# Kernel tuning notes

Hardware: AMD Instinct MI355X
Metric: run time of the kernel (lower is better)

## Reference

```python
import jax, jax.numpy as jnp
import numpy as np

C = 1.0      # base manifold curvature (Lorentz c)
C_E = 1.0    # expert manifold curvature (all experts init to c=1.0)
K = 1        # n_activated_experts (top-k)
SCALE = 2.0  # LResNet scale for shared-expert combine
EPS = 1e-8


def _lorentz_swiglu(x, W1, W3, W2, c_mid, c_out, prescale):
    """LorentzExpert / LorentzFeedForward: SwiGLU on space coords with Lorentz time lift.
    x: [T, D] (full Lorentz vector). W1,W3: [I-1, D]; W2: [D-1, I]. Returns [T, D]."""
    if prescale:
        x = x * np.float32(np.sqrt(C_E / C))  # x * sqrt(c_expert / c)
    s1 = jax.nn.silu(x @ W1.T)                 # [T, I-1] w1(x, return_space=True)
    s3 = x @ W3.T                              # [T, I-1] w3(x, return_space=True)
    sp = s1 * s3                               # gated space part
    t = jnp.sqrt(jnp.clip((sp * sp).sum(-1, keepdims=True) + c_mid, EPS))
    h = jnp.concatenate([t, sp], axis=-1)      # [T, I] point on expert manifold
    o = h @ W2.T                               # [T, D-1] w2 space output
    ot = jnp.sqrt(jnp.clip((o * o).sum(-1, keepdims=True) + c_out, EPS))
    return jnp.concatenate([ot, o], axis=-1)   # [T, D] on base manifold


def setup_inputs() -> dict:
    key = jax.random.key(0)
    ks = jax.random.split(key, 9)
    T, D, E, I = 2048, 1024, 8, 1024
    x = jax.random.normal(ks[0], (T, D), jnp.float32)
    gate_w = jax.random.normal(ks[1], (E, D - 1), jnp.float32) / np.sqrt(D - 1)
    gate_b = jax.random.normal(ks[2], (E,), jnp.float32) * 0.01
    W1 = jax.random.normal(ks[3], (E, I - 1, D), jnp.float32) / np.sqrt(D)
    W3 = jax.random.normal(ks[4], (E, I - 1, D), jnp.float32) / np.sqrt(D)
    W2 = jax.random.normal(ks[5], (E, D - 1, I), jnp.float32) / np.sqrt(I)
    Ws1 = jax.random.normal(ks[6], (I - 1, D), jnp.float32) / np.sqrt(D)
    Ws3 = jax.random.normal(ks[7], (I - 1, D), jnp.float32) / np.sqrt(D)
    Ws2 = jax.random.normal(ks[8], (D - 1, I), jnp.float32) / np.sqrt(I)
    return {"x": x, "gate_w": gate_w, "gate_b": gate_b, "W1": W1, "W3": W3,
            "W2": W2, "Ws1": Ws1, "Ws3": Ws3, "Ws2": Ws2}


def reference(x, gate_w, gate_b, W1, W3, W2, Ws1, Ws3, Ws2):
    T, D = x.shape
    E = gate_w.shape[0]
    # ---- Gate (softmax scoring, n_groups == 1, route_scale == 1.0) ----
    logits = x[:, 1:] @ gate_w.T                                    # [T, E]
    scores = jax.nn.softmax(logits.astype(jnp.float32), axis=-1)
    biased = scores + gate_b                                        # bias only affects routing
    _, idx = jax.lax.top_k(biased, K)                               # [T, K]
    weights = jnp.take_along_axis(scores, idx, axis=-1).astype(x.dtype)  # [T, K]
    # dense per-token expert gate weights [T, E]
    oh = jax.nn.one_hot(idx, E, dtype=x.dtype)                      # [T, K, E]
    gw = (oh * weights[..., None]).sum(axis=1)                      # [T, E]
    # ---- y init: project(zeros) -> [sqrt(c), 0, ..., 0] ----
    y0 = jnp.concatenate([jnp.full((T, 1), np.sqrt(C), x.dtype),
                          jnp.zeros((T, D - 1), x.dtype)], axis=-1)
    # ---- routed experts (dense reference: every expert on every token, masked combine) ----
    e_out = jax.vmap(lambda w1, w3, w2: _lorentz_swiglu(x, w1, w3, w2, C_E, C, True))(W1, W3, W2)  # [E, T, D]
    y = y0 + jnp.einsum('te,etd->td', gw, e_out)
    # ---- shared expert (LorentzFeedForward, stays on base manifold) ----
    z = _lorentz_swiglu(x, Ws1, Ws3, Ws2, C, C, False)
    # ---- LResNet weighted sum: normalize (z + scale*y) back to manifold ----
    comb = z + SCALE * y
    li = (comb[:, 1:] ** 2).sum(-1, keepdims=True) - comb[:, :1] ** 2  # Lorentz inner <comb,comb>
    out = np.float32(np.sqrt(C)) * comb / jnp.sqrt(jnp.clip(jnp.abs(li), EPS))
    return out
```

## Files before the change

### kernel.cpp

```cpp
#include <hip/hip_runtime.h>

typedef __bf16 bf16;
typedef __attribute__((ext_vector_type(8))) __bf16 bf16x8;
typedef __attribute__((ext_vector_type(4))) float floatx4;

#define TOK 2048
#define DD  1024
#define NE  8
#define LDA 40
#define MAXSLOT 72

__device__ __forceinline__ uint4 pack_bf8(float4 a, float4 b) {
  union { bf16 h[8]; uint4 u; } p;
  p.h[0] = (bf16)a.x; p.h[1] = (bf16)a.y; p.h[2] = (bf16)a.z; p.h[3] = (bf16)a.w;
  p.h[4] = (bf16)b.x; p.h[5] = (bf16)b.y; p.h[6] = (bf16)b.z; p.h[7] = (bf16)b.w;
  return p.u;
}

__global__ __launch_bounds__(256) void gate_cvt_kernel(
    const float* __restrict__ x, const float* __restrict__ gate_w,
    const float* __restrict__ gate_b, bf16* __restrict__ x_bf,
    int* __restrict__ eidx, float* __restrict__ ewgt)
{
  const int t = blockIdx.x, tid = threadIdx.x;
  const float4 v = ((const float4*)(x + (size_t)t * DD))[tid];
  union { bf16 h[4]; uint2 u; } pk;
  pk.h[0] = (bf16)v.x; pk.h[1] = (bf16)v.y; pk.h[2] = (bf16)v.z; pk.h[3] = (bf16)v.w;
  ((uint2*)(x_bf + (size_t)t * DD))[tid] = pk.u;

  float acc[NE];
#pragma unroll
  for (int e = 0; e < NE; ++e) acc[e] = 0.f;
  const float vv[4] = {v.x, v.y, v.z, v.w};
#pragma unroll
  for (int i = 0; i < 4; ++i) {
    const int d = tid * 4 + i;
    if (d >= 1) {
#pragma unroll
      for (int e = 0; e < NE; ++e) acc[e] += vv[i] * gate_w[e * (DD - 1) + d - 1];
    }
  }
#pragma unroll
  for (int off = 32; off > 0; off >>= 1) {
#pragma unroll
    for (int e = 0; e < NE; ++e) acc[e] += __shfl_down(acc[e], off);
  }
  __shared__ float red[4][NE];
  const int wid = tid >> 6, lane = tid & 63;
  if (lane == 0) {
#pragma unroll
    for (int e = 0; e < NE; ++e) red[wid][e] = acc[e];
  }
  __syncthreads();
  if (tid == 0) {
    float lg[NE];
#pragma unroll
    for (int e = 0; e < NE; ++e) lg[e] = red[0][e] + red[1][e] + red[2][e] + red[3][e];
    float m = lg[0];
    for (int e = 1; e < NE; ++e) m = fmaxf(m, lg[e]);
    float ex[NE], s = 0.f;
    for (int e = 0; e < NE; ++e) { ex[e] = expf(lg[e] - m); s += ex[e]; }
    const float inv = 1.f / s;
    int best = 0; float bb = ex[0] * inv + gate_b[0];
    for (int e = 1; e < NE; ++e) {
      const float b = ex[e] * inv + gate_b[e];
      if (b > bb) { bb = b; best = e; }
    }
    eidx[t] = best;
    ewgt[t] = ex[best] * inv;
  }
}

__global__ __launch_bounds__(256) void route_kernel(
    const int* __restrict__ eidx, int* __restrict__ perm,
    int* __restrict__ pos_of, int4* __restrict__ wl, int* __restrict__ wl_n)
{
  __shared__ int cnt[NE], off[NE], bas[NE + 1];
  const int tid = threadIdx.x;
  if (tid < NE) cnt[tid] = 0;
  __syncthreads();
  for (int t = tid; t < TOK; t += 256) atomicAdd(&cnt[eidx[t]], 1);
  __syncthreads();
  if (tid == 0) {
    int run = 0;
    for (int e = 0; e < NE; ++e) { bas[e] = run; off[e] = run; run += cnt[e]; }
    bas[NE] = run;
    int n = 0;
    for (int e = 0; e < NE; ++e)
      for (int r0 = 0; r0 < cnt[e]; r0 += 64) {
        int rows = cnt[e] - r0; if (rows > 64) rows = 64;
        wl[n++] = make_int4(bas[e] + r0, rows, e, 0);
      }
    for (int r0 = 0; r0 < TOK; r0 += 64) wl[n++] = make_int4(r0, 64, NE, 0);
    *wl_n = n;
  }
  __syncthreads();
  for (int t = tid; t < TOK; t += 256) {
    const int e = eidx[t];
    const int p = atomicAdd(&off[e], 1);
    perm[p] = t;
    pos_of[t] = p;
  }
}

__global__ __launch_bounds__(256) void mlp1_kernel(
    const bf16* __restrict__ x_bf,
    const float* __restrict__ W1, const float* __restrict__ W3,
    const float* __restrict__ Ws1, const float* __restrict__ Ws3,
    const int* __restrict__ perm, const int4* __restrict__ wl,
    const int* __restrict__ wl_n,
    bf16* __restrict__ h_r, bf16* __restrict__ h_s,
    float* __restrict__ ss_r, float* __restrict__ ss_z)
{
  const int bid = blockIdx.x;
  const int slot = bid >> 4, nt = bid & 15;
  if (slot >= *wl_n) return;
  const int4 wle = wl[slot];
  const int mbase = wle.x, rows = wle.y, eid = wle.z;
  const int tid = threadIdx.x;
  const bool routed = (eid < NE);
  const float* w1p = routed ? W1 + (size_t)eid * 1023 * 1024 : Ws1;
  const float* w3p = routed ? W3 + (size_t)eid * 1023 * 1024 : Ws3;
  bf16* hbuf  = routed ? h_r : h_s;
  float* ssbuf = routed ? ss_r : ss_z;
  const int n0 = nt * 64;

  __shared__ __align__(16) bf16 As[64 * LDA];
  __shared__ __align__(16) bf16 B1s[64 * LDA];
  __shared__ __align__(16) bf16 B3s[64 * LDA];
  __shared__ int toks[64];

  if (tid < 64) {
    int r = tid < rows ? tid : rows - 1;
    toks[tid] = routed ? perm[mbase + r] : (mbase + r);
  }
  __syncthreads();

  const int arow = tid >> 2, acol = (tid & 3) * 8;
  const bf16* aptr = x_bf + (size_t)toks[arow] * DD + acol;
  bf16* const alds = As + arow * LDA + acol;

  const int brow = tid >> 2, bcol = (tid & 3) * 8;
  int bn = n0 + brow; if (bn > 1022) bn = 1022;
  const float* b1ptr = w1p + (size_t)bn * 1024 + bcol;
  const float* b3ptr = w3p + (size_t)bn * 1024 + bcol;
  bf16* const b1lds = B1s + brow * LDA + bcol;
  bf16* const b3lds = B3s + brow * LDA + bcol;

  const int wid = tid >> 6, lane = tid & 63;
  const int wc = wid * 16;
  const int lrow = lane & 15, quad = lane >> 4;

  const floatx4 fz = {0.f, 0.f, 0.f, 0.f};
  floatx4 acc1[4], acc3[4];
#pragma unroll
  for (int mi = 0; mi < 4; ++mi) { acc1[mi] = fz; acc3[mi] = fz; }

  uint4  a0  = *(const uint4*)(aptr);
  float4 f10 = *(const float4*)(b1ptr);
  float4 f11 = *(const float4*)(b1ptr + 4);
  float4 f30 = *(const float4*)(b3ptr);
  float4 f31 = *(const float4*)(b3ptr + 4);

  for (int k0 = 0; k0 < 1024; k0 += 32) {
    __syncthreads();
    *(uint4*)alds  = a0;
    *(uint4*)b1lds = pack_bf8(f10, f11);
    *(uint4*)b3lds = pack_bf8(f30, f31);
    __syncthreads();
    const int kn = (k0 + 32 < 1024) ? (k0 + 32) : 0;
    a0  = *(const uint4*)(aptr + kn);
    f10 = *(const float4*)(b1ptr + kn);
    f11 = *(const float4*)(b1ptr + kn + 4);
    f30 = *(const float4*)(b3ptr + kn);
    f31 = *(const float4*)(b3ptr + kn + 4);

    bf16x8 af[4], b1f, b3f;
#pragma unroll
    for (int mi = 0; mi < 4; ++mi)
      af[mi] = *(const bf16x8*)(As + (mi * 16 + lrow) * LDA + quad * 8);
    b1f = *(const bf16x8*)(B1s + (wc + lrow) * LDA + quad * 8);
    b3f = *(const bf16x8*)(B3s + (wc + lrow) * LDA + quad * 8);
#pragma unroll
    for (int mi = 0; mi < 4; ++mi) {
      acc1[mi] = __builtin_amdgcn_mfma_f32_16x16x32_bf16(af[mi], b1f, acc1[mi], 0, 0, 0);
      acc3[mi] = __builtin_amdgcn_mfma_f32_16x16x32_bf16(af[mi], b3f, acc3[mi], 0, 0, 0);
    }
  }

  const int n = n0 + wc + lrow;
#pragma unroll
  for (int mi = 0; mi < 4; ++mi) {
#pragma unroll
    for (int r = 0; r < 4; ++r) {
      const int row = mi * 16 + quad * 4 + r;
      const bool ok = (row < rows) && (n < 1023);
      const float s1 = acc1[mi][r];
      const float s3 = acc3[mi][r];
      const float sp = (s1 / (1.f + __expf(-s1))) * s3;
      float ssum = ok ? sp * sp : 0.f;
      if (ok) hbuf[(size_t)(mbase + row) * 1024 + 1 + n] = (bf16)sp;
      ssum += __shfl_xor(ssum, 1);
      ssum += __shfl_xor(ssum, 2);
      ssum += __shfl_xor(ssum, 4);
      ssum += __shfl_xor(ssum, 8);
      if (lrow == 0 && row < rows) atomicAdd(ssbuf + mbase + row, ssum);
    }
  }
}

__global__ __launch_bounds__(256) void finalize_t_kernel(
    const float* __restrict__ ss_r, const float* __restrict__ ss_z,
    bf16* __restrict__ h_r, bf16* __restrict__ h_s)
{
  const int i = blockIdx.x * 256 + threadIdx.x;
  if (i < TOK) {
    h_r[(size_t)i * 1024] = (bf16)sqrtf(ss_r[i] + 1.0f);
    h_s[(size_t)i * 1024] = (bf16)sqrtf(ss_z[i] + 1.0f);
  }
}

__global__ __launch_bounds__(256) void mlp2_kernel(
    const bf16* __restrict__ h_r, const bf16* __restrict__ h_s,
    const float* __restrict__ W2, const float* __restrict__ Ws2,
    const int4* __restrict__ wl, const int* __restrict__ wl_n,
    float* __restrict__ o_r, float* __restrict__ o_s,
    float* __restrict__ ss_or, float* __restrict__ ss_oz)
{
  const int bid = blockIdx.x;
  const int slot = bid >> 4, nt = bid & 15;
  if (slot >= *wl_n) return;
  const int4 wle = wl[slot];
  const int mbase = wle.x, rows = wle.y, eid = wle.z;
  const int tid = threadIdx.x;
  const bool routed = (eid < NE);
  const float* wp = routed ? W2 + (size_t)eid * 1023 * 1024 : Ws2;
  const bf16* abuf = routed ? h_r : h_s;
  float* obuf  = routed ? o_r : o_s;
  float* ssbuf = routed ? ss_or : ss_oz;
  const int n0 = nt * 64;

  __shared__ __align__(16) bf16 As[64 * LDA];
  __shared__ __align__(16) bf16 Bs[64 * LDA];

  const int arow = tid >> 2, acol = (tid & 3) * 8;
  const int ar = arow < rows ? arow : rows - 1;
  const bf16* aptr = abuf + (size_t)(mbase + ar) * 1024 + acol;
  bf16* const alds = As + arow * LDA + acol;

  const int brow = tid >> 2, bcol = (tid & 3) * 8;
  int bn = n0 + brow; if (bn > 1022) bn = 1022;
  const float* bptr = wp + (size_t)bn * 1024 + bcol;
  bf16* const blds = Bs + brow * LDA + bcol;

  const int wid = tid >> 6, lane = tid & 63;
  const int wc = wid * 16;
  const int lrow = lane & 15, quad = lane >> 4;

  const floatx4 fz = {0.f, 0.f, 0.f, 0.f};
  floatx4 acc[4];
#pragma unroll
  for (int mi = 0; mi < 4; ++mi) acc[mi] = fz;

  uint4  a0 = *(const uint4*)(aptr);
  float4 f0 = *(const float4*)(bptr);
  float4 f1 = *(const float4*)(bptr + 4);

  for (int k0 = 0; k0 < 1024; k0 += 32) {
    __syncthreads();
    *(uint4*)alds = a0;
    *(uint4*)blds = pack_bf8(f0, f1);
    __syncthreads();
    const int kn = (k0 + 32 < 1024) ? (k0 + 32) : 0;
    a0 = *(const uint4*)(aptr + kn);
    f0 = *(const float4*)(bptr + kn);
    f1 = *(const float4*)(bptr + kn + 4);

    bf16x8 af[4], bfr;
#pragma unroll
    for (int mi = 0; mi < 4; ++mi)
      af[mi] = *(const bf16x8*)(As + (mi * 16 + lrow) * LDA + quad * 8);
    bfr = *(const bf16x8*)(Bs + (wc + lrow) * LDA + quad * 8);
#pragma unroll
    for (int mi = 0; mi < 4; ++mi)
      acc[mi] = __builtin_amdgcn_mfma_f32_16x16x32_bf16(af[mi], bfr, acc[mi], 0, 0, 0);
  }

  const int n = n0 + wc + lrow;
#pragma unroll
  for (int mi = 0; mi < 4; ++mi) {
#pragma unroll
    for (int r = 0; r < 4; ++r) {
      const int row = mi * 16 + quad * 4 + r;
      const bool ok = (row < rows) && (n < 1023);
      const float v = acc[mi][r];
      float ssum = ok ? v * v : 0.f;
      if (ok) obuf[(size_t)(mbase + row) * 1024 + n] = v;
      ssum += __shfl_xor(ssum, 1);
      ssum += __shfl_xor(ssum, 2);
      ssum += __shfl_xor(ssum, 4);
      ssum += __shfl_xor(ssum, 8);
      if (lrow == 0 && row < rows) atomicAdd(ssbuf + mbase + row, ssum);
    }
  }
}

__global__ __launch_bounds__(256) void combine_kernel(
    const float* __restrict__ o_r, const float* __restrict__ o_s,
    const float* __restrict__ ss_or, const float* __restrict__ ss_oz,
    const int* __restrict__ pos_of, const float* __restrict__ wgt,
    float* __restrict__ out)
{
  const int t = blockIdx.x, tid = threadIdx.x;
  const int p = pos_of[t];
  const float w = wgt[t];
  const float4 oz = ((const float4*)(o_s + (size_t)t * 1024))[tid];
  const float4 oe = ((const float4*)(o_r + (size_t)p * 1024))[tid];
  const float tw = 2.f * w;
  float c0 = oz.x + tw * oe.x;
  float c1 = oz.y + tw * oe.y;
  float c2 = oz.z + tw * oe.z;
  float c3 = (tid == 255) ? 0.f : (oz.w + tw * oe.w);
  float ssum = c0 * c0 + c1 * c1 + c2 * c2 + c3 * c3;
#pragma unroll
  for (int off = 32; off > 0; off >>= 1) ssum += __shfl_down(ssum, off);
  __shared__ float rs[4];
  if ((tid & 63) == 0) rs[tid >> 6] = ssum;
  __syncthreads();
  const float space2 = rs[0] + rs[1] + rs[2] + rs[3];
  const float comb0 = sqrtf(ss_oz[t] + 1.f) + 2.f + 2.f * w * sqrtf(ss_or[p] + 1.f);
  const float li = space2 - comb0 * comb0;
  const float inv = 1.f / sqrtf(fmaxf(fabsf(li), 1e-8f));
  float* orow = out + (size_t)t * 1024;
  const int j = 1 + tid * 4;
  orow[j]     = c0 * inv;
  orow[j + 1] = c1 * inv;
  orow[j + 2] = c2 * inv;
  if (tid != 255) orow[j + 3] = c3 * inv;
  if (tid == 0) orow[0] = comb0 * inv;
}

extern "C" void kernel_launch(void* const* d_in, const int* in_sizes, int n_in,
                              void* d_out, int out_size, void* d_ws, size_t ws_size,
                              hipStream_t stream) {
  const float* x      = (const float*)d_in[0];
  const float* gate_w = (const float*)d_in[1];
  const float* gate_b = (const float*)d_in[2];
  const float* W1     = (const float*)d_in[3];
  const float* W3     = (const float*)d_in[4];
  const float* W2     = (const float*)d_in[5];
  const float* Ws1    = (const float*)d_in[6];
  const float* Ws3    = (const float*)d_in[7];
  const float* Ws2    = (const float*)d_in[8];
  float* out = (float*)d_out;

  char* ws = (char*)d_ws;
  size_t off = 0;
  auto alloc = [&](size_t bytes) {
    void* p = ws + off;
    off += (bytes + 255) & ~(size_t)255;
    return p;
  };
  bf16*  x_bf = (bf16*) alloc((size_t)TOK * 1024 * 2);
  bf16*  h_r  = (bf16*) alloc((size_t)TOK * 1024 * 2);
  bf16*  h_s  = (bf16*) alloc((size_t)TOK * 1024 * 2);
  float* o_r  = (float*)alloc((size_t)TOK * 1024 * 4);
  float* o_s  = (float*)alloc((size_t)TOK * 1024 * 4);
  float* ss   = (float*)alloc((size_t)4 * TOK * 4);
  int*   eidx = (int*)  alloc((size_t)TOK * 4);
  float* ewgt = (float*)alloc((size_t)TOK * 4);
  int*   perm = (int*)  alloc((size_t)TOK * 4);
  int*   posf = (int*)  alloc((size_t)TOK * 4);
  int4*  wl   = (int4*) alloc((size_t)MAXSLOT * 16);
  int*   wln  = (int*)  alloc(16);

  float* ss_r  = ss;
  float* ss_z  = ss + TOK;
  float* ss_or = ss + 2 * TOK;
  float* ss_oz = ss + 3 * TOK;

  hipMemsetAsync(ss, 0, (size_t)4 * TOK * 4, stream);
  gate_cvt_kernel<<<TOK, 256, 0, stream>>>(x, gate_w, gate_b, x_bf, eidx, ewgt);
  route_kernel<<<1, 256, 0, stream>>>(eidx, perm, posf, wl, wln);
  mlp1_kernel<<<MAXSLOT * 16, 256, 0, stream>>>(x_bf, W1, W3, Ws1, Ws3, perm, wl, wln,
                                                h_r, h_s, ss_r, ss_z);
  finalize_t_kernel<<<8, 256, 0, stream>>>(ss_r, ss_z, h_r, h_s);
  mlp2_kernel<<<MAXSLOT * 16, 256, 0, stream>>>(h_r, h_s, W2, Ws2, wl, wln,
                                                o_r, o_s, ss_or, ss_oz);
  combine_kernel<<<TOK, 256, 0, stream>>>(o_r, o_s, ss_or, ss_oz, posf, ewgt, out);
}
```

Baseline: 285.1 us.

## Double-buffer LDS tiles in both MLP GEMM kernels with one barrier per step

Both expert GEMM kernels switch from a single LDS tile with two barriers per K step to ping-pong LDS buffers with a single barrier. Global loads are issued two tiles ahead in registers, and the store for the next tile overlaps the MFMA work on the current one. The goal is to cut barrier stalls and hide global load latency. In exchange it doubles LDS use and adds register pressure from the extra prefetch registers, which could reduce occupancy.

```diff
diff --git a/kernel.cpp b/kernel.cpp
--- a/kernel.cpp
+++ b/kernel.cpp
@@ -125,9 +125,9 @@
   float* ssbuf = routed ? ss_r : ss_z;
   const int n0 = nt * 64;
 
-  __shared__ __align__(16) bf16 As[64 * LDA];
-  __shared__ __align__(16) bf16 B1s[64 * LDA];
-  __shared__ __align__(16) bf16 B3s[64 * LDA];
+  __shared__ __align__(16) bf16 As[2][64 * LDA];
+  __shared__ __align__(16) bf16 B1s[2][64 * LDA];
+  __shared__ __align__(16) bf16 B3s[2][64 * LDA];
   __shared__ int toks[64];
 
   if (tid < 64) {
@@ -138,14 +138,13 @@
 
   const int arow = tid >> 2, acol = (tid & 3) * 8;
   const bf16* aptr = x_bf + (size_t)toks[arow] * DD + acol;
-  bf16* const alds = As + arow * LDA + acol;
+  const int aoff = arow * LDA + acol;
 
   const int brow = tid >> 2, bcol = (tid & 3) * 8;
   int bn = n0 + brow; if (bn > 1022) bn = 1022;
   const float* b1ptr = w1p + (size_t)bn * 1024 + bcol;
   const float* b3ptr = w3p + (size_t)bn * 1024 + bcol;
-  bf16* const b1lds = B1s + brow * LDA + bcol;
-  bf16* const b3lds = B3s + brow * LDA + bcol;
+  const int boff = brow * LDA + bcol;
 
   const int wid = tid >> 6, lane = tid & 63;
   const int wc = wid * 16;
@@ -156,37 +155,53 @@
 #pragma unroll
   for (int mi = 0; mi < 4; ++mi) { acc1[mi] = fz; acc3[mi] = fz; }
 
-  uint4  a0  = *(const uint4*)(aptr);
-  float4 f10 = *(const float4*)(b1ptr);
-  float4 f11 = *(const float4*)(b1ptr + 4);
-  float4 f30 = *(const float4*)(b3ptr);
-  float4 f31 = *(const float4*)(b3ptr + 4);
-
-  for (int k0 = 0; k0 < 1024; k0 += 32) {
-    __syncthreads();
-    *(uint4*)alds  = a0;
-    *(uint4*)b1lds = pack_bf8(f10, f11);
-    *(uint4*)b3lds = pack_bf8(f30, f31);
-    __syncthreads();
-    const int kn = (k0 + 32 < 1024) ? (k0 + 32) : 0;
-    a0  = *(const uint4*)(aptr + kn);
-    f10 = *(const float4*)(b1ptr + kn);
-    f11 = *(const float4*)(b1ptr + kn + 4);
-    f30 = *(const float4*)(b3ptr + kn);
-    f31 = *(const float4*)(b3ptr + kn + 4);
-
-    bf16x8 af[4], b1f, b3f;
-#pragma unroll
-    for (int mi = 0; mi < 4; ++mi)
-      af[mi] = *(const bf16x8*)(As + (mi * 16 + lrow) * LDA + quad * 8);
-    b1f = *(const bf16x8*)(B1s + (wc + lrow) * LDA + quad * 8);
-    b3f = *(const bf16x8*)(B3s + (wc + lrow) * LDA + quad * 8);
-#pragma unroll
-    for (int mi = 0; mi < 4; ++mi) {
-      acc1[mi] = __builtin_amdgcn_mfma_f32_16x16x32_bf16(af[mi], b1f, acc1[mi], 0, 0, 0);
-      acc3[mi] = __builtin_amdgcn_mfma_f32_16x16x32_bf16(af[mi], b3f, acc3[mi], 0, 0, 0);
-    }
-  }
+  uint4  ra0, ra1; float4 r10_0, r11_0, r30_0, r31_0, r10_1, r11_1, r30_1, r31_1;
+  ra0 = *(const uint4*)(aptr);
+  r10_0 = *(const float4*)(b1ptr);     r11_0 = *(const float4*)(b1ptr + 4);
+  r30_0 = *(const float4*)(b3ptr);     r31_0 = *(const float4*)(b3ptr + 4);
+  ra1 = *(const uint4*)(aptr + 32);
+  r10_1 = *(const float4*)(b1ptr + 32); r11_1 = *(const float4*)(b1ptr + 36);
+  r30_1 = *(const float4*)(b3ptr + 32); r31_1 = *(const float4*)(b3ptr + 36);
+  *(uint4*)(&As[0][aoff])  = ra0;
+  *(uint4*)(&B1s[0][boff]) = pack_bf8(r10_0, r11_0);
+  *(uint4*)(&B3s[0][boff]) = pack_bf8(r30_0, r31_0);
+  ra0 = *(const uint4*)(aptr + 64);
+  r10_0 = *(const float4*)(b1ptr + 64); r11_0 = *(const float4*)(b1ptr + 68);
+  r30_0 = *(const float4*)(b3ptr + 64); r31_0 = *(const float4*)(b3ptr + 68);
+
+#define MLP1_STEP(KK, CUR, NXT, RA, R10, R11, R30, R31)                              \
+  {                                                                                  \
+    __syncthreads();                                                                 \
+    bf16x8 af0 = *(const bf16x8*)(&As[CUR][(0 * 16 + lrow) * LDA + quad * 8]);       \
+    bf16x8 af1 = *(const bf16x8*)(&As[CUR][(1 * 16 + lrow) * LDA + quad * 8]);       \
+    bf16x8 af2 = *(const bf16x8*)(&As[CUR][(2 * 16 + lrow) * LDA + quad * 8]);       \
+    bf16x8 af3 = *(const bf16x8*)(&As[CUR][(3 * 16 + lrow) * LDA + quad * 8]);       \
+    bf16x8 b1f = *(const bf16x8*)(&B1s[CUR][(wc + lrow) * LDA + quad * 8]);          \
+    bf16x8 b3f = *(const bf16x8*)(&B3s[CUR][(wc + lrow) * LDA + quad * 8]);          \
+    if ((KK) < 31) {                                                                 \
+      *(uint4*)(&As[NXT][aoff])  = RA;                                               \
+      *(uint4*)(&B1s[NXT][boff]) = pack_bf8(R10, R11);                               \
+      *(uint4*)(&B3s[NXT][boff]) = pack_bf8(R30, R31);                               \
+      const int kt = ((KK) + 3 < 32 ? (KK) + 3 : 0) * 32;                            \
+      RA  = *(const uint4*)(aptr + kt);                                              \
+      R10 = *(const float4*)(b1ptr + kt); R11 = *(const float4*)(b1ptr + kt + 4);    \
+      R30 = *(const float4*)(b3ptr + kt); R31 = *(const float4*)(b3ptr + kt + 4);    \
+    }                                                                                \
+    acc1[0] = __builtin_amdgcn_mfma_f32_16x16x32_bf16(af0, b1f, acc1[0], 0, 0, 0);   \
+    acc3[0] = __builtin_amdgcn_mfma_f32_16x16x32_bf16(af0, b3f, acc3[0], 0, 0, 0);   \
+    acc1[1] = __builtin_amdgcn_mfma_f32_16x16x32_bf16(af1, b1f, acc1[1], 0, 0, 0);   \
+    acc3[1] = __builtin_amdgcn_mfma_f32_16x16x32_bf16(af1, b3f, acc3[1], 0, 0, 0);   \
+    acc1[2] = __builtin_amdgcn_mfma_f32_16x16x32_bf16(af2, b1f, acc1[2], 0, 0, 0);   \
+    acc3[2] = __builtin_amdgcn_mfma_f32_16x16x32_bf16(af2, b3f, acc3[2], 0, 0, 0);   \
+    acc1[3] = __builtin_amdgcn_mfma_f32_16x16x32_bf16(af3, b1f, acc1[3], 0, 0, 0);   \
+    acc3[3] = __builtin_amdgcn_mfma_f32_16x16x32_bf16(af3, b3f, acc3[3], 0, 0, 0);   \
+  }
+
+  for (int k = 0; k < 32; k += 2) {
+    MLP1_STEP(k,     0, 1, ra1, r10_1, r11_1, r30_1, r31_1);
+    MLP1_STEP(k + 1, 1, 0, ra0, r10_0, r11_0, r30_0, r31_0);
+  }
+#undef MLP1_STEP
 
   const int n = n0 + wc + lrow;
 #pragma unroll
@@ -240,18 +255,18 @@
   float* ssbuf = routed ? ss_or : ss_oz;
   const int n0 = nt * 64;
 
-  __shared__ __align__(16) bf16 As[64 * LDA];
-  __shared__ __align__(16) bf16 Bs[64 * LDA];
+  __shared__ __align__(16) bf16 As[2][64 * LDA];
+  __shared__ __align__(16) bf16 Bs[2][64 * LDA];
 
   const int arow = tid >> 2, acol = (tid & 3) * 8;
   const int ar = arow < rows ? arow : rows - 1;
   const bf16* aptr = abuf + (size_t)(mbase + ar) * 1024 + acol;
-  bf16* const alds = As + arow * LDA + acol;
+  const int aoff = arow * LDA + acol;
 
   const int brow = tid >> 2, bcol = (tid & 3) * 8;
   int bn = n0 + brow; if (bn > 1022) bn = 1022;
   const float* bptr = wp + (size_t)bn * 1024 + bcol;
-  bf16* const blds = Bs + brow * LDA + bcol;
+  const int boff = brow * LDA + bcol;
 
   const int wid = tid >> 6, lane = tid & 63;
   const int wc = wid * 16;
@@ -262,29 +277,42 @@
 #pragma unroll
   for (int mi = 0; mi < 4; ++mi) acc[mi] = fz;
 
-  uint4  a0 = *(const uint4*)(aptr);
-  float4 f0 = *(const float4*)(bptr);
-  float4 f1 = *(const float4*)(bptr + 4);
-
-  for (int k0 = 0; k0 < 1024; k0 += 32) {
-    __syncthreads();
-    *(uint4*)alds = a0;
-    *(uint4*)blds = pack_bf8(f0, f1);
-    __syncthreads();
-    const int kn = (k0 + 32 < 1024) ? (k0 + 32) : 0;
-    a0 = *(const uint4*)(aptr + kn);
-    f0 = *(const float4*)(bptr + kn);
-    f1 = *(const float4*)(bptr + kn + 4);
-
-    bf16x8 af[4], bfr;
-#pragma unroll
-    for (int mi = 0; mi < 4; ++mi)
-      af[mi] = *(const bf16x8*)(As + (mi * 16 + lrow) * LDA + quad * 8);
-    bfr = *(const bf16x8*)(Bs + (wc + lrow) * LDA + quad * 8);
-#pragma unroll
-    for (int mi = 0; mi < 4; ++mi)
-      acc[mi] = __builtin_amdgcn_mfma_f32_16x16x32_bf16(af[mi], bfr, acc[mi], 0, 0, 0);
-  }
+  uint4 ra0, ra1; float4 r0_0, r1_0, r0_1, r1_1;
+  ra0 = *(const uint4*)(aptr);
+  r0_0 = *(const float4*)(bptr);      r1_0 = *(const float4*)(bptr + 4);
+  ra1 = *(const uint4*)(aptr + 32);
+  r0_1 = *(const float4*)(bptr + 32); r1_1 = *(const float4*)(bptr + 36);
+  *(uint4*)(&As[0][aoff]) = ra0;
+  *(uint4*)(&Bs[0][boff]) = pack_bf8(r0_0, r1_0);
+  ra0 = *(const uint4*)(aptr + 64);
+  r0_0 = *(const float4*)(bptr + 64); r1_0 = *(const float4*)(bptr + 68);
+
+#define MLP2_STEP(KK, CUR, NXT, RA, R0, R1)                                          \
+  {                                                                                  \
+    __syncthreads();                                                                 \
+    bf16x8 af0 = *(const bf16x8*)(&As[CUR][(0 * 16 + lrow) * LDA + quad * 8]);       \
+    bf16x8 af1 = *(const bf16x8*)(&As[CUR][(1 * 16 + lrow) * LDA + quad * 8]);       \
+    bf16x8 af2 = *(const bf16x8*)(&As[CUR][(2 * 16 + lrow) * LDA + quad * 8]);       \
+    bf16x8 af3 = *(const bf16x8*)(&As[CUR][(3 * 16 + lrow) * LDA + quad * 8]);       \
+    bf16x8 bfr = *(const bf16x8*)(&Bs[CUR][(wc + lrow) * LDA + quad * 8]);           \
+    if ((KK) < 31) {                                                                 \
+      *(uint4*)(&As[NXT][aoff]) = RA;                                                \
+      *(uint4*)(&Bs[NXT][boff]) = pack_bf8(R0, R1);                                  \
+      const int kt = ((KK) + 3 < 32 ? (KK) + 3 : 0) * 32;                            \
+      RA = *(const uint4*)(aptr + kt);                                               \
+      R0 = *(const float4*)(bptr + kt); R1 = *(const float4*)(bptr + kt + 4);        \
+    }                                                                                \
+    acc[0] = __builtin_amdgcn_mfma_f32_16x16x32_bf16(af0, bfr, acc[0], 0, 0, 0);     \
+    acc[1] = __builtin_amdgcn_mfma_f32_16x16x32_bf16(af1, bfr, acc[1], 0, 0, 0);     \
+    acc[2] = __builtin_amdgcn_mfma_f32_16x16x32_bf16(af2, bfr, acc[2], 0, 0, 0);     \
+    acc[3] = __builtin_amdgcn_mfma_f32_16x16x32_bf16(af3, bfr, acc[3], 0, 0, 0);     \
+  }
+
+  for (int k = 0; k < 32; k += 2) {
+    MLP2_STEP(k,     0, 1, ra1, r0_1, r1_1);
+    MLP2_STEP(k + 1, 1, 0, ra0, r0_0, r1_0);
+  }
+#undef MLP2_STEP
 
   const int n = n0 + wc + lrow;
 #pragma unroll
```

After: 283.5 us. No clear change (-0.6%).

## Load GEMM fragments directly from global into registers, drop LDS staging and extra launches

Applied to the files above, without the earlier changes.

Both MLP GEMM kernels stop staging A and B tiles through shared memory with two barriers per k-step. Each lane now loads its MFMA fragments straight from global memory into registers, using a 4-deep software-pipelined register ring. The memset is folded into the gate kernel, and the time-coordinate finalize kernel is removed by computing sqrt(ss+1) inside mlp2 and patching it into the first A fragment. The trade-off is that data is no longer shared across waves: each wave re-reads the A rows and weight rows from global or L2 with less coalesced 16-byte per-lane accesses, and register pressure rises.

```diff
diff --git a/kernel.cpp b/kernel.cpp
--- a/kernel.cpp
+++ b/kernel.cpp
@@ -7,22 +7,24 @@
 #define TOK 2048
 #define DD  1024
 #define NE  8
-#define LDA 40
 #define MAXSLOT 72
 
-__device__ __forceinline__ uint4 pack_bf8(float4 a, float4 b) {
-  union { bf16 h[8]; uint4 u; } p;
+#define MFMA16(A,B,C) __builtin_amdgcn_mfma_f32_16x16x32_bf16(A,B,C,0,0,0)
+
+__device__ __forceinline__ bf16x8 pack_bf8v(float4 a, float4 b) {
+  union { bf16 h[8]; bf16x8 v; } p;
   p.h[0] = (bf16)a.x; p.h[1] = (bf16)a.y; p.h[2] = (bf16)a.z; p.h[3] = (bf16)a.w;
   p.h[4] = (bf16)b.x; p.h[5] = (bf16)b.y; p.h[6] = (bf16)b.z; p.h[7] = (bf16)b.w;
-  return p.u;
+  return p.v;
 }
 
 __global__ __launch_bounds__(256) void gate_cvt_kernel(
     const float* __restrict__ x, const float* __restrict__ gate_w,
     const float* __restrict__ gate_b, bf16* __restrict__ x_bf,
-    int* __restrict__ eidx, float* __restrict__ ewgt)
+    int* __restrict__ eidx, float* __restrict__ ewgt, float* __restrict__ ss)
 {
   const int t = blockIdx.x, tid = threadIdx.x;
+  if (tid < 4) ss[tid * TOK + t] = 0.f;
   const float4 v = ((const float4*)(x + (size_t)t * DD))[tid];
   union { bf16 h[4]; uint2 u; } pk;
   pk.h[0] = (bf16)v.x; pk.h[1] = (bf16)v.y; pk.h[2] = (bf16)v.z; pk.h[3] = (bf16)v.w;
@@ -125,68 +127,58 @@
   float* ssbuf = routed ? ss_r : ss_z;
   const int n0 = nt * 64;
 
-  __shared__ __align__(16) bf16 As[64 * LDA];
-  __shared__ __align__(16) bf16 B1s[64 * LDA];
-  __shared__ __align__(16) bf16 B3s[64 * LDA];
   __shared__ int toks[64];
-
   if (tid < 64) {
     int r = tid < rows ? tid : rows - 1;
     toks[tid] = routed ? perm[mbase + r] : (mbase + r);
   }
   __syncthreads();
 
-  const int arow = tid >> 2, acol = (tid & 3) * 8;
-  const bf16* aptr = x_bf + (size_t)toks[arow] * DD + acol;
-  bf16* const alds = As + arow * LDA + acol;
-
-  const int brow = tid >> 2, bcol = (tid & 3) * 8;
-  int bn = n0 + brow; if (bn > 1022) bn = 1022;
-  const float* b1ptr = w1p + (size_t)bn * 1024 + bcol;
-  const float* b3ptr = w3p + (size_t)bn * 1024 + bcol;
-  bf16* const b1lds = B1s + brow * LDA + bcol;
-  bf16* const b3lds = B3s + brow * LDA + bcol;
-
   const int wid = tid >> 6, lane = tid & 63;
   const int wc = wid * 16;
   const int lrow = lane & 15, quad = lane >> 4;
 
+  const bf16* aP0 = x_bf + (size_t)toks[ 0 + lrow] * DD + quad * 8;
+  const bf16* aP1 = x_bf + (size_t)toks[16 + lrow] * DD + quad * 8;
+  const bf16* aP2 = x_bf + (size_t)toks[32 + lrow] * DD + quad * 8;
+  const bf16* aP3 = x_bf + (size_t)toks[48 + lrow] * DD + quad * 8;
+
+  int bn = n0 + wc + lrow; if (bn > 1022) bn = 1022;
+  const float* b1P = w1p + (size_t)bn * 1024 + quad * 8;
+  const float* b3P = w3p + (size_t)bn * 1024 + quad * 8;
+
   const floatx4 fz = {0.f, 0.f, 0.f, 0.f};
   floatx4 acc1[4], acc3[4];
 #pragma unroll
   for (int mi = 0; mi < 4; ++mi) { acc1[mi] = fz; acc3[mi] = fz; }
 
-  uint4  a0  = *(const uint4*)(aptr);
-  float4 f10 = *(const float4*)(b1ptr);
-  float4 f11 = *(const float4*)(b1ptr + 4);
-  float4 f30 = *(const float4*)(b3ptr);
-  float4 f31 = *(const float4*)(b3ptr + 4);
-
-  for (int k0 = 0; k0 < 1024; k0 += 32) {
-    __syncthreads();
-    *(uint4*)alds  = a0;
-    *(uint4*)b1lds = pack_bf8(f10, f11);
-    *(uint4*)b3lds = pack_bf8(f30, f31);
-    __syncthreads();
-    const int kn = (k0 + 32 < 1024) ? (k0 + 32) : 0;
-    a0  = *(const uint4*)(aptr + kn);
-    f10 = *(const float4*)(b1ptr + kn);
-    f11 = *(const float4*)(b1ptr + kn + 4);
-    f30 = *(const float4*)(b3ptr + kn);
-    f31 = *(const float4*)(b3ptr + kn + 4);
-
-    bf16x8 af[4], b1f, b3f;
-#pragma unroll
-    for (int mi = 0; mi < 4; ++mi)
-      af[mi] = *(const bf16x8*)(As + (mi * 16 + lrow) * LDA + quad * 8);
-    b1f = *(const bf16x8*)(B1s + (wc + lrow) * LDA + quad * 8);
-    b3f = *(const bf16x8*)(B3s + (wc + lrow) * LDA + quad * 8);
-#pragma unroll
-    for (int mi = 0; mi < 4; ++mi) {
-      acc1[mi] = __builtin_amdgcn_mfma_f32_16x16x32_bf16(af[mi], b1f, acc1[mi], 0, 0, 0);
-      acc3[mi] = __builtin_amdgcn_mfma_f32_16x16x32_bf16(af[mi], b3f, acc3[mi], 0, 0, 0);
-    }
-  }
+#define LDA4(D,K) { D[0] = *(const bf16x8*)(aP0 + (K)); D[1] = *(const bf16x8*)(aP1 + (K)); \
+                    D[2] = *(const bf16x8*)(aP2 + (K)); D[3] = *(const bf16x8*)(aP3 + (K)); }
+#define LDB4(D,K) { D[0] = *(const float4*)(b1P + (K)); D[1] = *(const float4*)(b1P + (K) + 4); \
+                    D[2] = *(const float4*)(b3P + (K)); D[3] = *(const float4*)(b3P + (K) + 4); }
+#define CMP1(A,B) { bf16x8 b1f = pack_bf8v(B[0], B[1]); bf16x8 b3f = pack_bf8v(B[2], B[3]); \
+  acc1[0] = MFMA16(A[0], b1f, acc1[0]); acc3[0] = MFMA16(A[0], b3f, acc3[0]); \
+  acc1[1] = MFMA16(A[1], b1f, acc1[1]); acc3[1] = MFMA16(A[1], b3f, acc3[1]); \
+  acc1[2] = MFMA16(A[2], b1f, acc1[2]); acc3[2] = MFMA16(A[2], b3f, acc3[2]); \
+  acc1[3] = MFMA16(A[3], b1f, acc1[3]); acc3[3] = MFMA16(A[3], b3f, acc3[3]); }
+
+  bf16x8 Aa[4], Ab[4], Ac[4], Ad[4];
+  float4 Ba[4], Bb[4], Bc[4], Bd[4];
+  LDA4(Aa, 0)  LDB4(Ba, 0)
+  LDA4(Ab, 32) LDB4(Bb, 32)
+  for (int k0 = 0; k0 < 1024; k0 += 128) {
+    LDA4(Ac, (k0 +  64) & 1023)  LDB4(Bc, (k0 +  64) & 1023)
+    CMP1(Aa, Ba)
+    LDA4(Ad, (k0 +  96) & 1023)  LDB4(Bd, (k0 +  96) & 1023)
+    CMP1(Ab, Bb)
+    LDA4(Aa, (k0 + 128) & 1023)  LDB4(Ba, (k0 + 128) & 1023)
+    CMP1(Ac, Bc)
+    LDA4(Ab, (k0 + 160) & 1023)  LDB4(Bb, (k0 + 160) & 1023)
+    CMP1(Ad, Bd)
+  }
+#undef LDA4
+#undef LDB4
+#undef CMP1
 
   const int n = n0 + wc + lrow;
 #pragma unroll
@@ -209,21 +201,11 @@
   }
 }
 
-__global__ __launch_bounds__(256) void finalize_t_kernel(
-    const float* __restrict__ ss_r, const float* __restrict__ ss_z,
-    bf16* __restrict__ h_r, bf16* __restrict__ h_s)
-{
-  const int i = blockIdx.x * 256 + threadIdx.x;
-  if (i < TOK) {
-    h_r[(size_t)i * 1024] = (bf16)sqrtf(ss_r[i] + 1.0f);
-    h_s[(size_t)i * 1024] = (bf16)sqrtf(ss_z[i] + 1.0f);
-  }
-}
-
 __global__ __launch_bounds__(256) void mlp2_kernel(
     const bf16* __restrict__ h_r, const bf16* __restrict__ h_s,
     const float* __restrict__ W2, const float* __restrict__ Ws2,
     const int4* __restrict__ wl, const int* __restrict__ wl_n,
+    const float* __restrict__ ss_r, const float* __restrict__ ss_z,
     float* __restrict__ o_r, float* __restrict__ o_s,
     float* __restrict__ ss_or, float* __restrict__ ss_oz)
 {
@@ -236,55 +218,60 @@
   const bool routed = (eid < NE);
   const float* wp = routed ? W2 + (size_t)eid * 1023 * 1024 : Ws2;
   const bf16* abuf = routed ? h_r : h_s;
+  const float* ssmid = routed ? ss_r : ss_z;
   float* obuf  = routed ? o_r : o_s;
   float* ssbuf = routed ? ss_or : ss_oz;
   const int n0 = nt * 64;
 
-  __shared__ __align__(16) bf16 As[64 * LDA];
-  __shared__ __align__(16) bf16 Bs[64 * LDA];
-
-  const int arow = tid >> 2, acol = (tid & 3) * 8;
-  const int ar = arow < rows ? arow : rows - 1;
-  const bf16* aptr = abuf + (size_t)(mbase + ar) * 1024 + acol;
-  bf16* const alds = As + arow * LDA + acol;
-
-  const int brow = tid >> 2, bcol = (tid & 3) * 8;
-  int bn = n0 + brow; if (bn > 1022) bn = 1022;
-  const float* bptr = wp + (size_t)bn * 1024 + bcol;
-  bf16* const blds = Bs + brow * LDA + bcol;
-
   const int wid = tid >> 6, lane = tid & 63;
   const int wc = wid * 16;
   const int lrow = lane & 15, quad = lane >> 4;
 
+  const bf16* aP[4];
+  float tv[4];
+#pragma unroll
+  for (int mi = 0; mi < 4; ++mi) {
+    int r = mi * 16 + lrow; if (r >= rows) r = rows - 1;
+    aP[mi] = abuf + (size_t)(mbase + r) * 1024 + quad * 8;
+    tv[mi] = sqrtf(ssmid[mbase + r] + 1.0f);
+  }
+
+  int bn = n0 + wc + lrow; if (bn > 1022) bn = 1022;
+  const float* bP = wp + (size_t)bn * 1024 + quad * 8;
+
   const floatx4 fz = {0.f, 0.f, 0.f, 0.f};
   floatx4 acc[4];
 #pragma unroll
   for (int mi = 0; mi < 4; ++mi) acc[mi] = fz;
 
-  uint4  a0 = *(const uint4*)(aptr);
-  float4 f0 = *(const float4*)(bptr);
-  float4 f1 = *(const float4*)(bptr + 4);
-
-  for (int k0 = 0; k0 < 1024; k0 += 32) {
-    __syncthreads();
-    *(uint4*)alds = a0;
-    *(uint4*)blds = pack_bf8(f0, f1);
-    __syncthreads();
-    const int kn = (k0 + 32 < 1024) ? (k0 + 32) : 0;
-    a0 = *(const uint4*)(aptr + kn);
-    f0 = *(const float4*)(bptr + kn);
-    f1 = *(const float4*)(bptr + kn + 4);
-
-    bf16x8 af[4], bfr;
-#pragma unroll
-    for (int mi = 0; mi < 4; ++mi)
-      af[mi] = *(const bf16x8*)(As + (mi * 16 + lrow) * LDA + quad * 8);
-    bfr = *(const bf16x8*)(Bs + (wc + lrow) * LDA + quad * 8);
-#pragma unroll
-    for (int mi = 0; mi < 4; ++mi)
-      acc[mi] = __builtin_amdgcn_mfma_f32_16x16x32_bf16(af[mi], bfr, acc[mi], 0, 0, 0);
-  }
+#define LDA4(D,K) { D[0] = *(const bf16x8*)(aP[0] + (K)); D[1] = *(const bf16x8*)(aP[1] + (K)); \
+                    D[2] = *(const bf16x8*)(aP[2] + (K)); D[3] = *(const bf16x8*)(aP[3] + (K)); }
+#define LDB2(D,K) { D[0] = *(const float4*)(bP + (K)); D[1] = *(const float4*)(bP + (K) + 4); }
+#define CMP2(A,B) { bf16x8 bfv = pack_bf8v(B[0], B[1]); \
+  acc[0] = MFMA16(A[0], bfv, acc[0]); acc[1] = MFMA16(A[1], bfv, acc[1]); \
+  acc[2] = MFMA16(A[2], bfv, acc[2]); acc[3] = MFMA16(A[3], bfv, acc[3]); }
+
+  bf16x8 Aa[4], Ab[4], Ac[4], Ad[4];
+  float4 Ba[2], Bb[2], Bc[2], Bd[2];
+  LDA4(Aa, 0)  LDB2(Ba, 0)
+  if (quad == 0) {
+#pragma unroll
+    for (int mi = 0; mi < 4; ++mi) Aa[mi][0] = (bf16)tv[mi];
+  }
+  LDA4(Ab, 32) LDB2(Bb, 32)
+  for (int k0 = 0; k0 < 1024; k0 += 128) {
+    LDA4(Ac, (k0 +  64) & 1023)  LDB2(Bc, (k0 +  64) & 1023)
+    CMP2(Aa, Ba)
+    LDA4(Ad, (k0 +  96) & 1023)  LDB2(Bd, (k0 +  96) & 1023)
+    CMP2(Ab, Bb)
+    LDA4(Aa, (k0 + 128) & 1023)  LDB2(Ba, (k0 + 128) & 1023)
+    CMP2(Ac, Bc)
+    LDA4(Ab, (k0 + 160) & 1023)  LDB2(Bb, (k0 + 160) & 1023)
+    CMP2(Ad, Bd)
+  }
+#undef LDA4
+#undef LDB2
+#undef CMP2
 
   const int n = n0 + wc + lrow;
 #pragma unroll
@@ -379,13 +366,11 @@
   float* ss_or = ss + 2 * TOK;
   float* ss_oz = ss + 3 * TOK;
 
-  hipMemsetAsync(ss, 0, (size_t)4 * TOK * 4, stream);
-  gate_cvt_kernel<<<TOK, 256, 0, stream>>>(x, gate_w, gate_b, x_bf, eidx, ewgt);
+  gate_cvt_kernel<<<TOK, 256, 0, stream>>>(x, gate_w, gate_b, x_bf, eidx, ewgt, ss);
   route_kernel<<<1, 256, 0, stream>>>(eidx, perm, posf, wl, wln);
   mlp1_kernel<<<MAXSLOT * 16, 256, 0, stream>>>(x_bf, W1, W3, Ws1, Ws3, perm, wl, wln,
                                                 h_r, h_s, ss_r, ss_z);
-  finalize_t_kernel<<<8, 256, 0, stream>>>(ss_r, ss_z, h_r, h_s);
   mlp2_kernel<<<MAXSLOT * 16, 256, 0, stream>>>(h_r, h_s, W2, Ws2, wl, wln,
-                                                o_r, o_s, ss_or, ss_oz);
+                                                ss_r, ss_z, o_r, o_s, ss_or, ss_oz);
   combine_kernel<<<TOK, 256, 0, stream>>>(o_r, o_s, ss_or, ss_oz, posf, ewgt, out);
 }
```

Result: slower. 493.5 us (+73.1%).
